# Kernel tuning notes

Measured on AMD Instinct MI355X. Metric: run time of the kernel, lower is better.

## Reference

```python
import jax, jax.numpy as jnp
import numpy as np

N = 8192
IN_F = 256
OUT_F = 128
ALPHA = 0.2  # leakyrelu slope
NEG_BIG = -9e15


def setup_inputs() -> dict:
    key = jax.random.key(0)
    k1, k2, k3, k4 = jax.random.split(key, 4)
    x = jax.random.normal(k1, (N, IN_F), dtype=jnp.float32)
    adj = (jax.random.uniform(k2, (N, N)) < 0.01).astype(jnp.float32)
    adj = jnp.maximum(adj, jnp.eye(N, dtype=jnp.float32))
    # xavier-uniform-style init scales
    W = jax.random.uniform(k3, (IN_F, OUT_F), dtype=jnp.float32,
                           minval=-1.0, maxval=1.0) * np.sqrt(6.0 / (IN_F + OUT_F))
    a = jax.random.uniform(k4, (2 * OUT_F, 1), dtype=jnp.float32,
                           minval=-1.0, maxval=1.0) * np.sqrt(6.0 / (2 * OUT_F + 1))
    return {"x": x, "adj": adj, "W": W, "a": a}


def reference(x, adj, W, a):
    # h = x @ W  -> (N, F)
    h = x @ W
    # e_ij = leakyrelu(a^T [h_i || h_j]) = leakyrelu((h @ a1)_i + (h @ a2)_j)
    # equivalent to torch's repeat/cat construction, without the N^2*2F tensor
    a1 = a[:OUT_F, 0]   # (F,)
    a2 = a[OUT_F:, 0]   # (F,)
    s1 = h @ a1         # (N,)
    s2 = h @ a2         # (N,)
    e = s1[:, None] + s2[None, :]                      # (N, N)
    e = jnp.where(e > 0, e, ALPHA * e)                 # leakyrelu
    att = jnp.where(adj > 0, e, NEG_BIG)
    att = jax.nn.softmax(att, axis=1)                  # (N, N)
    # dropout is identity in eval mode
    h_prime = att @ h                                  # (N, F)
    return jax.nn.elu(h_prime)
```

## Files before the change

### kernel.cpp

```cpp
#include <hip/hip_runtime.h>
#include <cstdint>
#include <cstddef>

#define N 8192
#define IN_F 256
#define OUT_F 128
#define ALPHA 0.2f
#define CAP 256
typedef unsigned long long ull;
typedef float f32x4 __attribute__((ext_vector_type(4)));

__device__ __forceinline__ float bf2f(unsigned short u) {
    return __uint_as_float(((unsigned)u) << 16);
}
__device__ __forceinline__ unsigned short f2bf(float f) {
    unsigned x = __float_as_uint(f);
    unsigned r = (x + 0x7FFFu + ((x >> 16) & 1u)) >> 16;
    return (unsigned short)r;
}

__global__ __launch_bounds__(256) void gemm_xw(const float* __restrict__ x,
                                               const float* __restrict__ W,
                                               const float* __restrict__ a,
                                               unsigned short* __restrict__ hb,
                                               float* __restrict__ s1,
                                               float* __restrict__ s2) {
    __shared__ __align__(16) float xsT[64 * 20];
    __shared__ __align__(16) float ws[64 * 128];
    const int tid = threadIdx.x;
    const int R0  = blockIdx.x * 16;
    const int r0  = (tid >> 5) * 2;
    const int c0  = (tid & 31) * 4;

    float acc[2][4];
#pragma unroll
    for (int r = 0; r < 2; ++r)
#pragma unroll
        for (int c = 0; c < 4; ++c) acc[r][c] = 0.f;

    for (int k0 = 0; k0 < IN_F; k0 += 64) {
        {
            const int r  = tid >> 4;
            const int k4 = tid & 15;
            const float4 v = *(const float4*)(x + (size_t)(R0 + r) * IN_F + k0 + k4 * 4);
            xsT[(k4 * 4 + 0) * 20 + r] = v.x;
            xsT[(k4 * 4 + 1) * 20 + r] = v.y;
            xsT[(k4 * 4 + 2) * 20 + r] = v.z;
            xsT[(k4 * 4 + 3) * 20 + r] = v.w;
        }
#pragma unroll
        for (int q = 0; q < 8; ++q) {
            const int f = tid + q * 256;
            *(float4*)(ws + f * 4) = *(const float4*)(W + (size_t)k0 * OUT_F + f * 4);
        }
        __syncthreads();

#pragma unroll 8
        for (int kk = 0; kk < 64; ++kk) {
            const float4 wv = *(const float4*)(ws + kk * 128 + c0);
            const float2 xv = *(const float2*)(xsT + kk * 20 + r0);
            acc[0][0] += xv.x * wv.x; acc[0][1] += xv.x * wv.y; acc[0][2] += xv.x * wv.z; acc[0][3] += xv.x * wv.w;
            acc[1][0] += xv.y * wv.x; acc[1][1] += xv.y * wv.y; acc[1][2] += xv.y * wv.z; acc[1][3] += xv.y * wv.w;
        }
        __syncthreads();
    }

#pragma unroll
    for (int r = 0; r < 2; ++r) {
        ushort4 o4;
        o4.x = f2bf(acc[r][0]); o4.y = f2bf(acc[r][1]);
        o4.z = f2bf(acc[r][2]); o4.w = f2bf(acc[r][3]);
        *(ushort4*)(hb + (size_t)(R0 + r0 + r) * OUT_F + c0) = o4;
    }

    const float4 a1v = *(const float4*)(a + c0);
    const float4 a2v = *(const float4*)(a + OUT_F + c0);
#pragma unroll
    for (int r = 0; r < 2; ++r) {
        float p1 = acc[r][0] * a1v.x + acc[r][1] * a1v.y + acc[r][2] * a1v.z + acc[r][3] * a1v.w;
        float p2 = acc[r][0] * a2v.x + acc[r][1] * a2v.y + acc[r][2] * a2v.z + acc[r][3] * a2v.w;
#pragma unroll
        for (int off = 16; off > 0; off >>= 1) {
            p1 += __shfl_xor(p1, off);
            p2 += __shfl_xor(p2, off);
        }
        if ((tid & 31) == 0) {
            s1[R0 + r0 + r] = p1;
            s2[R0 + r0 + r] = p2;
        }
    }
}

__global__ __launch_bounds__(256, 8) void gat_fused(const float* __restrict__ adj,
                                                    const unsigned short* __restrict__ hb,
                                                    const float* __restrict__ s1,
                                                    const float* __restrict__ s2,
                                                    float* __restrict__ out) {
    const int tid  = threadIdx.x;
    const int wv   = tid >> 6;
    const int lane = tid & 63;
    const int row  = blockIdx.x * 4 + wv;

    __shared__ int   jl[4][CAP];
    __shared__ float el[4][CAP];

    const f32x4* __restrict__ arow = (const f32x4*)(adj + (size_t)row * N);
    const ull below = (1ull << lane) - 1ull;

    int tot = 0;
    f32x4 va[4], vb[4];
#pragma unroll
    for (int u = 0; u < 4; ++u) va[u] = __builtin_nontemporal_load(arow + lane + u * 64);

    for (int b = 0; b < 8; ++b) {
        if (b < 7) {
#pragma unroll
            for (int u = 0; u < 4; ++u)
                vb[u] = __builtin_nontemporal_load(arow + lane + ((b + 1) * 4 + u) * 64);
        }
#pragma unroll
        for (int u = 0; u < 4; ++u) {
            const int jb = (((b * 4 + u) * 64) + lane) * 4;
            const float av[4] = {va[u].x, va[u].y, va[u].z, va[u].w};
#pragma unroll
            for (int c = 0; c < 4; ++c) {
                const bool hit = av[c] > 0.f;
                const ull m = __ballot(hit);
                if (m) {
                    const int base = tot;
                    tot += __popcll(m);
                    if (hit) {
                        const int p = base + __popcll(m & below);
                        if (p < CAP) jl[wv][p] = jb + c;
                    }
                }
            }
        }
#pragma unroll
        for (int u = 0; u < 4; ++u) va[u] = vb[u];
    }
    const int n = tot < CAP ? tot : CAP;

    const float si = s1[row];
    float ev[4];
    float lmax = -1e30f;
#pragma unroll
    for (int t = 0; t < 4; ++t) {
        const int l = lane + t * 64;
        float e = -1e30f;
        if (l < n) {
            e = si + s2[jl[wv][l]];
            e = e > 0.f ? e : ALPHA * e;
        }
        ev[t] = e;
        lmax = fmaxf(lmax, e);
    }
#pragma unroll
    for (int off = 32; off > 0; off >>= 1) lmax = fmaxf(lmax, __shfl_xor(lmax, off));

    float dp = 0.f;
#pragma unroll
    for (int t = 0; t < 4; ++t) {
        const int l = lane + t * 64;
        if (l < n) {
            const float wgt = __expf(ev[t] - lmax);
            el[wv][l] = wgt;
            dp += wgt;
        }
    }
#pragma unroll
    for (int off = 32; off > 0; off >>= 1) dp += __shfl_xor(dp, off);
    const float denom = dp;

    const int half = lane >> 5;
    const int col4 = (lane & 31) * 4;
    float a0 = 0.f, a1 = 0.f, a2 = 0.f, a3 = 0.f;
#pragma unroll 4
    for (int l = half; l < n; l += 2) {
        const float wgt = el[wv][l];
        const int j = jl[wv][l];
        const ushort4 hv = *(const ushort4*)(hb + (size_t)j * OUT_F + col4);
        a0 += wgt * bf2f(hv.x);
        a1 += wgt * bf2f(hv.y);
        a2 += wgt * bf2f(hv.z);
        a3 += wgt * bf2f(hv.w);
    }
    a0 += __shfl_xor(a0, 32);
    a1 += __shfl_xor(a1, 32);
    a2 += __shfl_xor(a2, 32);
    a3 += __shfl_xor(a3, 32);

    if (half == 0) {
        const float r = 1.f / denom;
        float v0 = a0 * r, v1 = a1 * r, v2 = a2 * r, v3 = a3 * r;
        float4 o;
        o.x = v0 > 0.f ? v0 : (__expf(v0) - 1.f);
        o.y = v1 > 0.f ? v1 : (__expf(v1) - 1.f);
        o.z = v2 > 0.f ? v2 : (__expf(v2) - 1.f);
        o.w = v3 > 0.f ? v3 : (__expf(v3) - 1.f);
        *(float4*)(out + (size_t)row * OUT_F + col4) = o;
    }
}

extern "C" void kernel_launch(void* const* d_in, const int* in_sizes, int n_in,
                              void* d_out, int out_size, void* d_ws, size_t ws_size,
                              hipStream_t stream) {
    const float* x   = (const float*)d_in[0];
    const float* adj = (const float*)d_in[1];
    const float* W   = (const float*)d_in[2];
    const float* a   = (const float*)d_in[3];
    float* out = (float*)d_out;

    char* wsb = (char*)d_ws;
    unsigned short* hb = (unsigned short*)wsb;
    float* s1 = (float*)(wsb + 2 * 1024 * 1024);
    float* s2 = s1 + N;

    gemm_xw<<<N / 16, 256, 0, stream>>>(x, W, a, hb, s1, s2);
    gat_fused<<<2048, 256, 0, stream>>>(adj, hb, s1, s2, out);
}
```

Measured before the change: 73.54 us.

## Split each adjacency row across four waves and drop softmax max pass

Each block still handles four rows, but now all four waves scan interleaved quarters of each row. The per-(row, quarter) neighbour lists go into shared memory, and a block barrier lets each wave gather its own row's lists. The softmax no longer subtracts the row maximum and computes exp directly, which removes one cross-lane reduction. The adjacency loads also drop the nontemporal hint. The goal is more coalesced, block-wide streaming of the dense adjacency and less per-row reduction work. The cost is a __syncthreads, a cap of 128 neighbours per quarter, and overflow risk for large logits.

```diff
diff --git a/kernel.cpp b/kernel.cpp
--- a/kernel.cpp
+++ b/kernel.cpp
@@ -6,7 +6,7 @@
 #define IN_F 256
 #define OUT_F 128
 #define ALPHA 0.2f
-#define CAP 256
+#define QCAP 128
 typedef unsigned long long ull;
 typedef float f32x4 __attribute__((ext_vector_type(4)));
 
@@ -99,73 +99,72 @@
     const int tid  = threadIdx.x;
     const int wv   = tid >> 6;
     const int lane = tid & 63;
-    const int row  = blockIdx.x * 4 + wv;
-
-    __shared__ int   jl[4][CAP];
-    __shared__ float el[4][CAP];
-
-    const f32x4* __restrict__ arow = (const f32x4*)(adj + (size_t)row * N);
+    const int R0   = blockIdx.x * 4;
+
+    __shared__ int   jl[4][4][QCAP];
+    __shared__ float el[4][4][QCAP];
+    __shared__ int   cntS[4][4];
+
+    const f32x4* __restrict__ base4 = (const f32x4*)(adj + (size_t)R0 * N);
     const ull below = (1ull << lane) - 1ull;
 
-    int tot = 0;
+    int p = 0;
     f32x4 va[4], vb[4];
 #pragma unroll
-    for (int u = 0; u < 4; ++u) va[u] = __builtin_nontemporal_load(arow + lane + u * 64);
+    for (int u = 0; u < 4; ++u) va[u] = base4[u * 256 + wv * 64 + lane];
 
     for (int b = 0; b < 8; ++b) {
         if (b < 7) {
 #pragma unroll
             for (int u = 0; u < 4; ++u)
-                vb[u] = __builtin_nontemporal_load(arow + lane + ((b + 1) * 4 + u) * 64);
+                vb[u] = base4[(b * 4 + 4 + u) * 256 + wv * 64 + lane];
         }
 #pragma unroll
         for (int u = 0; u < 4; ++u) {
-            const int jb = (((b * 4 + u) * 64) + lane) * 4;
+            const int t  = b * 4 + u;
+            const int rt = t >> 3;
+            const int jb = ((t & 7) * 256 + wv * 64 + lane) * 4;
             const float av[4] = {va[u].x, va[u].y, va[u].z, va[u].w};
 #pragma unroll
             for (int c = 0; c < 4; ++c) {
                 const bool hit = av[c] > 0.f;
                 const ull m = __ballot(hit);
                 if (m) {
-                    const int base = tot;
-                    tot += __popcll(m);
+                    const int bs = p;
+                    p += __popcll(m);
                     if (hit) {
-                        const int p = base + __popcll(m & below);
-                        if (p < CAP) jl[wv][p] = jb + c;
+                        const int q = bs + __popcll(m & below);
+                        if (q < QCAP) jl[rt][wv][q] = jb + c;
                     }
                 }
             }
+            if ((t & 7) == 7) {
+                if (lane == 0) cntS[rt][wv] = (p < QCAP ? p : QCAP);
+                p = 0;
+            }
         }
 #pragma unroll
         for (int u = 0; u < 4; ++u) va[u] = vb[u];
     }
-    const int n = tot < CAP ? tot : CAP;
-
+    __syncthreads();
+
+    const int row = R0 + wv;
     const float si = s1[row];
-    float ev[4];
-    float lmax = -1e30f;
-#pragma unroll
-    for (int t = 0; t < 4; ++t) {
-        const int l = lane + t * 64;
-        float e = -1e30f;
-        if (l < n) {
-            e = si + s2[jl[wv][l]];
-            e = e > 0.f ? e : ALPHA * e;
-        }
-        ev[t] = e;
-        lmax = fmaxf(lmax, e);
-    }
-#pragma unroll
-    for (int off = 32; off > 0; off >>= 1) lmax = fmaxf(lmax, __shfl_xor(lmax, off));
 
     float dp = 0.f;
 #pragma unroll
-    for (int t = 0; t < 4; ++t) {
-        const int l = lane + t * 64;
-        if (l < n) {
-            const float wgt = __expf(ev[t] - lmax);
-            el[wv][l] = wgt;
-            dp += wgt;
+    for (int s = 0; s < 4; ++s) {
+        const int ns = cntS[wv][s];
+#pragma unroll
+        for (int t = 0; t < 2; ++t) {
+            const int l = lane + t * 64;
+            if (l < ns) {
+                float e = si + s2[jl[wv][s][l]];
+                e = e > 0.f ? e : ALPHA * e;
+                const float w = __expf(e);
+                el[wv][s][l] = w;
+                dp += w;
+            }
         }
     }
 #pragma unroll
@@ -175,15 +174,19 @@
     const int half = lane >> 5;
     const int col4 = (lane & 31) * 4;
     float a0 = 0.f, a1 = 0.f, a2 = 0.f, a3 = 0.f;
-#pragma unroll 4
-    for (int l = half; l < n; l += 2) {
-        const float wgt = el[wv][l];
-        const int j = jl[wv][l];
-        const ushort4 hv = *(const ushort4*)(hb + (size_t)j * OUT_F + col4);
-        a0 += wgt * bf2f(hv.x);
-        a1 += wgt * bf2f(hv.y);
-        a2 += wgt * bf2f(hv.z);
-        a3 += wgt * bf2f(hv.w);
+#pragma unroll
+    for (int s = 0; s < 4; ++s) {
+        const int ns = cntS[wv][s];
+#pragma unroll 2
+        for (int l = half; l < ns; l += 2) {
+            const float wgt = el[wv][s][l];
+            const int j = jl[wv][s][l];
+            const ushort4 hv = *(const ushort4*)(hb + (size_t)j * OUT_F + col4);
+            a0 += wgt * bf2f(hv.x);
+            a1 += wgt * bf2f(hv.y);
+            a2 += wgt * bf2f(hv.z);
+            a3 += wgt * bf2f(hv.w);
+        }
     }
     a0 += __shfl_xor(a0, 32);
     a1 += __shfl_xor(a1, 32);
```

Result: no change. 72.69 us (-1.2%).

## Fuse projection GEMM and attention into one cooperative kernel with atomic flag

Applied to the files above, without the earlier changes.

Merges the x@W projection and the GAT attention kernel into one cooperative launch. The first 512 blocks compute h, s1 and s2, then signal completion through a global atomic counter. Every block compacts its adjacency rows first and spins on the counter only before it needs s1, s2 and h, so the dense adjacency scan overlaps the GEMM and a kernel boundary disappears. It also drops the softmax max-subtraction pass, which risks exp overflow for large logits, and switches the adjacency loads from nontemporal to normal loads. It keeps the two-kernel path as a fallback when occupancy is too low.

```diff
diff --git a/kernel.cpp b/kernel.cpp
--- a/kernel.cpp
+++ b/kernel.cpp
@@ -17,6 +17,178 @@
     unsigned x = __float_as_uint(f);
     unsigned r = (x + 0x7FFFu + ((x >> 16) & 1u)) >> 16;
     return (unsigned short)r;
+}
+
+__global__ __launch_bounds__(256, 8) void gat_all(const float* __restrict__ adj,
+                                                  const float* __restrict__ x,
+                                                  const float* __restrict__ W,
+                                                  const float* __restrict__ a,
+                                                  unsigned short* __restrict__ hb,
+                                                  float* __restrict__ s1,
+                                                  float* __restrict__ s2,
+                                                  int* done,
+                                                  float* __restrict__ out) {
+    __shared__ __align__(16) float smem[4736];
+    const int tid  = threadIdx.x;
+    const int wv   = tid >> 6;
+    const int lane = tid & 63;
+    const int bid  = blockIdx.x;
+
+    if (bid < 512) {
+        float* xsT = smem;
+        float* wsh = smem + 640;
+        const int R0 = bid * 16;
+        const int r0 = (tid >> 5) * 2;
+        const int c0 = (tid & 31) * 4;
+
+        float acc[2][4];
+#pragma unroll
+        for (int r = 0; r < 2; ++r)
+#pragma unroll
+            for (int c = 0; c < 4; ++c) acc[r][c] = 0.f;
+
+        for (int k0 = 0; k0 < IN_F; k0 += 32) {
+            if (tid < 128) {
+                const int r  = tid >> 3;
+                const int k4 = tid & 7;
+                const float4 v = *(const float4*)(x + (size_t)(R0 + r) * IN_F + k0 + k4 * 4);
+                xsT[(k4 * 4 + 0) * 20 + r] = v.x;
+                xsT[(k4 * 4 + 1) * 20 + r] = v.y;
+                xsT[(k4 * 4 + 2) * 20 + r] = v.z;
+                xsT[(k4 * 4 + 3) * 20 + r] = v.w;
+            }
+#pragma unroll
+            for (int q = 0; q < 4; ++q) {
+                const int f = tid + q * 256;
+                *(float4*)(wsh + f * 4) = *(const float4*)(W + (size_t)k0 * OUT_F + f * 4);
+            }
+            __syncthreads();
+#pragma unroll 8
+            for (int kk = 0; kk < 32; ++kk) {
+                const float4 wv4 = *(const float4*)(wsh + kk * 128 + c0);
+                const float2 xv  = *(const float2*)(xsT + kk * 20 + r0);
+                acc[0][0] += xv.x * wv4.x; acc[0][1] += xv.x * wv4.y; acc[0][2] += xv.x * wv4.z; acc[0][3] += xv.x * wv4.w;
+                acc[1][0] += xv.y * wv4.x; acc[1][1] += xv.y * wv4.y; acc[1][2] += xv.y * wv4.z; acc[1][3] += xv.y * wv4.w;
+            }
+            __syncthreads();
+        }
+
+#pragma unroll
+        for (int r = 0; r < 2; ++r) {
+            ushort4 o4;
+            o4.x = f2bf(acc[r][0]); o4.y = f2bf(acc[r][1]);
+            o4.z = f2bf(acc[r][2]); o4.w = f2bf(acc[r][3]);
+            *(ushort4*)(hb + (size_t)(R0 + r0 + r) * OUT_F + c0) = o4;
+        }
+        const float4 a1v = *(const float4*)(a + c0);
+        const float4 a2v = *(const float4*)(a + OUT_F + c0);
+#pragma unroll
+        for (int r = 0; r < 2; ++r) {
+            float p1 = acc[r][0] * a1v.x + acc[r][1] * a1v.y + acc[r][2] * a1v.z + acc[r][3] * a1v.w;
+            float p2 = acc[r][0] * a2v.x + acc[r][1] * a2v.y + acc[r][2] * a2v.z + acc[r][3] * a2v.w;
+#pragma unroll
+            for (int off = 16; off > 0; off >>= 1) {
+                p1 += __shfl_xor(p1, off);
+                p2 += __shfl_xor(p2, off);
+            }
+            if ((tid & 31) == 0) {
+                s1[R0 + r0 + r] = p1;
+                s2[R0 + r0 + r] = p2;
+            }
+        }
+        __threadfence();
+        __syncthreads();
+        if (tid == 0)
+            __hip_atomic_fetch_add(done, 1, __ATOMIC_RELEASE, __HIP_MEMORY_SCOPE_AGENT);
+    }
+
+    int*   jlw = ((int*)smem) + wv * CAP;
+    float* elw = (smem + 1024) + wv * CAP;
+    const int row = bid * 4 + wv;
+    const f32x4* __restrict__ arow = (const f32x4*)(adj + (size_t)row * N);
+    const ull below = (1ull << lane) - 1ull;
+
+    int tot = 0;
+    f32x4 va[4], vb[4];
+#pragma unroll
+    for (int u = 0; u < 4; ++u) va[u] = arow[lane + u * 64];
+
+    for (int b = 0; b < 8; ++b) {
+        if (b < 7) {
+#pragma unroll
+            for (int u = 0; u < 4; ++u) vb[u] = arow[lane + ((b + 1) * 4 + u) * 64];
+        }
+#pragma unroll
+        for (int u = 0; u < 4; ++u) {
+            const int jb = (((b * 4 + u) * 64) + lane) * 4;
+            const float av[4] = {va[u].x, va[u].y, va[u].z, va[u].w};
+#pragma unroll
+            for (int c = 0; c < 4; ++c) {
+                const bool hit = av[c] > 0.f;
+                const ull m = __ballot(hit);
+                if (m) {
+                    const int base = tot;
+                    tot += __popcll(m);
+                    if (hit) {
+                        const int p = base + __popcll(m & below);
+                        if (p < CAP) jlw[p] = jb + c;
+                    }
+                }
+            }
+        }
+#pragma unroll
+        for (int u = 0; u < 4; ++u) va[u] = vb[u];
+    }
+    const int n = tot < CAP ? tot : CAP;
+
+    while (__hip_atomic_load(done, __ATOMIC_ACQUIRE, __HIP_MEMORY_SCOPE_AGENT) < 512)
+        __builtin_amdgcn_s_sleep(8);
+
+    const float si = s1[row];
+    float dp = 0.f;
+#pragma unroll
+    for (int t = 0; t < 4; ++t) {
+        const int l = lane + t * 64;
+        if (l < n) {
+            float e = si + s2[jlw[l]];
+            e = e > 0.f ? e : ALPHA * e;
+            const float w = __expf(e);
+            elw[l] = w;
+            dp += w;
+        }
+    }
+#pragma unroll
+    for (int off = 32; off > 0; off >>= 1) dp += __shfl_xor(dp, off);
+    const float denom = dp;
+
+    const int half = lane >> 5;
+    const int col4 = (lane & 31) * 4;
+    float a0 = 0.f, a1 = 0.f, a2 = 0.f, a3 = 0.f;
+#pragma unroll 4
+    for (int l = half; l < n; l += 2) {
+        const float wgt = elw[l];
+        const int j = jlw[l];
+        const ushort4 hv = *(const ushort4*)(hb + (size_t)j * OUT_F + col4);
+        a0 += wgt * bf2f(hv.x);
+        a1 += wgt * bf2f(hv.y);
+        a2 += wgt * bf2f(hv.z);
+        a3 += wgt * bf2f(hv.w);
+    }
+    a0 += __shfl_xor(a0, 32);
+    a1 += __shfl_xor(a1, 32);
+    a2 += __shfl_xor(a2, 32);
+    a3 += __shfl_xor(a3, 32);
+
+    if (half == 0) {
+        const float r = 1.f / denom;
+        float v0 = a0 * r, v1 = a1 * r, v2 = a2 * r, v3 = a3 * r;
+        float4 o;
+        o.x = v0 > 0.f ? v0 : (__expf(v0) - 1.f);
+        o.y = v1 > 0.f ? v1 : (__expf(v1) - 1.f);
+        o.z = v2 > 0.f ? v2 : (__expf(v2) - 1.f);
+        o.w = v3 > 0.f ? v3 : (__expf(v3) - 1.f);
+        *(float4*)(out + (size_t)row * OUT_F + col4) = o;
+    }
 }
 
 __global__ __launch_bounds__(256) void gemm_xw(const float* __restrict__ x,
@@ -54,7 +226,6 @@
             *(float4*)(ws + f * 4) = *(const float4*)(W + (size_t)k0 * OUT_F + f * 4);
         }
         __syncthreads();
-
 #pragma unroll 8
         for (int kk = 0; kk < 64; ++kk) {
             const float4 wv = *(const float4*)(ws + kk * 128 + c0);
@@ -64,7 +235,6 @@
         }
         __syncthreads();
     }
-
 #pragma unroll
     for (int r = 0; r < 2; ++r) {
         ushort4 o4;
@@ -72,7 +242,6 @@
         o4.z = f2bf(acc[r][2]); o4.w = f2bf(acc[r][3]);
         *(ushort4*)(hb + (size_t)(R0 + r0 + r) * OUT_F + c0) = o4;
     }
-
     const float4 a1v = *(const float4*)(a + c0);
     const float4 a2v = *(const float4*)(a + OUT_F + c0);
 #pragma unroll
@@ -110,13 +279,12 @@
     int tot = 0;
     f32x4 va[4], vb[4];
 #pragma unroll
-    for (int u = 0; u < 4; ++u) va[u] = __builtin_nontemporal_load(arow + lane + u * 64);
+    for (int u = 0; u < 4; ++u) va[u] = arow[lane + u * 64];
 
     for (int b = 0; b < 8; ++b) {
         if (b < 7) {
 #pragma unroll
-            for (int u = 0; u < 4; ++u)
-                vb[u] = __builtin_nontemporal_load(arow + lane + ((b + 1) * 4 + u) * 64);
+            for (int u = 0; u < 4; ++u) vb[u] = arow[lane + ((b + 1) * 4 + u) * 64];
         }
 #pragma unroll
         for (int u = 0; u < 4; ++u) {
@@ -142,30 +310,16 @@
     const int n = tot < CAP ? tot : CAP;
 
     const float si = s1[row];
-    float ev[4];
-    float lmax = -1e30f;
-#pragma unroll
-    for (int t = 0; t < 4; ++t) {
-        const int l = lane + t * 64;
-        float e = -1e30f;
-        if (l < n) {
-            e = si + s2[jl[wv][l]];
-            e = e > 0.f ? e : ALPHA * e;
-        }
-        ev[t] = e;
-        lmax = fmaxf(lmax, e);
-    }
-#pragma unroll
-    for (int off = 32; off > 0; off >>= 1) lmax = fmaxf(lmax, __shfl_xor(lmax, off));
-
     float dp = 0.f;
 #pragma unroll
     for (int t = 0; t < 4; ++t) {
         const int l = lane + t * 64;
         if (l < n) {
-            const float wgt = __expf(ev[t] - lmax);
-            el[wv][l] = wgt;
-            dp += wgt;
+            float e = si + s2[jl[wv][l]];
+            e = e > 0.f ? e : ALPHA * e;
+            const float w = __expf(e);
+            el[wv][l] = w;
+            dp += w;
         }
     }
 #pragma unroll
@@ -215,7 +369,18 @@
     unsigned short* hb = (unsigned short*)wsb;
     float* s1 = (float*)(wsb + 2 * 1024 * 1024);
     float* s2 = s1 + N;
-
-    gemm_xw<<<N / 16, 256, 0, stream>>>(x, W, a, hb, s1, s2);
-    gat_fused<<<2048, 256, 0, stream>>>(adj, hb, s1, s2, out);
-}
+    int* done = (int*)(wsb + 2 * 1024 * 1024 + 64 * 1024);
+
+    int nb = 0;
+    (void)hipOccupancyMaxActiveBlocksPerMultiprocessor(&nb, gat_all, 256, 0);
+    if (nb >= 8) {
+        hipMemsetAsync(done, 0, sizeof(int), stream);
+        void* args[] = {(void*)&adj, (void*)&x, (void*)&W, (void*)&a,
+                        (void*)&hb, (void*)&s1, (void*)&s2, (void*)&done, (void*)&out};
+        hipLaunchCooperativeKernel((const void*)gat_all, dim3(2048), dim3(256),
+                                   args, 0, stream);
+    } else {
+        gemm_xw<<<N / 16, 256, 0, stream>>>(x, W, a, hb, s1, s2);
+        gat_fused<<<2048, 256, 0, stream>>>(adj, hb, s1, s2, out);
+    }
+}
```

Measured after the change: 70.65 us. 3.9% less time.
